# Performance work log

Hardware: AMD Instinct MI355X
Metric: run time of the kernel (lower is better)

Reference implementation:

```python
import jax, jax.numpy as jnp
import numpy as np
from jax import lax

DIM = 192
NUM_CLASSES = 4
D_INNER = 2 * DIM          # expand=2
D_STATE = 16
D_CONV = 4
DT_RANK = (DIM + 15) // 16  # ceil(192/16)=12
PATCH = 16


def _mamba_params(key, prefix):
    ks = jax.random.split(key, 9)
    s = lambda k, shape, scale: (jax.random.normal(k, shape, jnp.float32) * scale)
    p = {
        prefix + '_in_w':   s(ks[0], (2 * D_INNER, DIM), 0.02),
        prefix + '_conv_w': s(ks[1], (D_INNER, D_CONV), 0.1),
        prefix + '_conv_b': jnp.zeros((D_INNER,), jnp.float32),
        prefix + '_xproj_w': s(ks[2], (DT_RANK + 2 * D_STATE, D_INNER), 0.02),
        prefix + '_dt_w':   s(ks[3], (D_INNER, DT_RANK), 0.1),
        prefix + '_dt_b':   s(ks[4], (D_INNER,), 0.1),
        # A_log init: log(1..d_state) broadcast over d_inner (mamba default)
        prefix + '_A_log':  jnp.broadcast_to(jnp.log(jnp.arange(1, D_STATE + 1, dtype=jnp.float32)), (D_INNER, D_STATE)) + 0.0,
        prefix + '_D':      jnp.ones((D_INNER,), jnp.float32),
        prefix + '_out_w':  s(ks[5], (DIM, D_INNER), 0.02),
    }
    return p


def setup_inputs() -> dict:
    key = jax.random.key(0)
    ks = jax.random.split(key, 8)
    inp = {
        'x': jax.random.normal(ks[0], (32, 3, 384, 384), jnp.float32),
        'patch_w': jax.random.normal(ks[1], (DIM, 3, PATCH, PATCH), jnp.float32) * 0.02,
        'patch_b': jnp.zeros((DIM,), jnp.float32),
        'ln_g': jnp.ones((DIM,), jnp.float32),
        'ln_b': jnp.zeros((DIM,), jnp.float32),
        'fc_w': jax.random.normal(ks[2], (NUM_CLASSES, DIM), jnp.float32) * 0.02,
        'fc_b': jnp.zeros((NUM_CLASSES,), jnp.float32),
    }
    inp.update(_mamba_params(ks[3], 'f'))
    inp.update(_mamba_params(ks[4], 'b'))
    return inp


def _layernorm(x, g, b, eps=1e-5):
    mu = jnp.mean(x, -1, keepdims=True)
    var = jnp.mean(jnp.square(x - mu), -1, keepdims=True)
    return (x - mu) * lax.rsqrt(var + eps) * g + b


def _mamba(x, in_w, conv_w, conv_b, xproj_w, dt_w, dt_b, A_log, Dskip, out_w):
    # x: [B, L, DIM]
    Bn, L, _ = x.shape
    xz = x @ in_w.T                                    # [B, L, 2*di]
    xi, z = jnp.split(xz, 2, axis=-1)
    # causal depthwise conv1d, kernel D_CONV, left pad
    xp = jnp.pad(xi, ((0, 0), (D_CONV - 1, 0), (0, 0)))
    xc = conv_b + sum(xp[:, k:k + L, :] * conv_w[:, k] for k in range(D_CONV))
    xc = jax.nn.silu(xc)                               # [B, L, di]
    proj = xc @ xproj_w.T                              # [B, L, dtr+2*ds]
    dt, Bm, Cm = jnp.split(proj, [DT_RANK, DT_RANK + D_STATE], axis=-1)
    dt = jax.nn.softplus(dt @ dt_w.T + dt_b)           # [B, L, di]
    A = -jnp.exp(A_log)                                # [di, ds]

    def step(h, inp):
        dt_t, B_t, C_t, x_t = inp                      # [B,di],[B,ds],[B,ds],[B,di]
        dA = jnp.exp(dt_t[:, :, None] * A)             # [B, di, ds]
        h = dA * h + (dt_t * x_t)[:, :, None] * B_t[:, None, :]
        y = jnp.einsum('bds,bs->bd', h, C_t)
        return h, y

    h0 = jnp.zeros((Bn, D_INNER, D_STATE), x.dtype)
    xs = (dt.transpose(1, 0, 2), Bm.transpose(1, 0, 2),
          Cm.transpose(1, 0, 2), xc.transpose(1, 0, 2))
    _, ys = lax.scan(step, h0, xs)                     # [L, B, di]
    y = ys.transpose(1, 0, 2) + xc * Dskip
    y = y * jax.nn.silu(z)
    return y @ out_w.T                                 # [B, L, DIM]


def reference(x, patch_w, patch_b, ln_g, ln_b, fc_w, fc_b,
              f_in_w, f_conv_w, f_conv_b, f_xproj_w, f_dt_w, f_dt_b, f_A_log, f_D, f_out_w,
              b_in_w, b_conv_w, b_conv_b, b_xproj_w, b_dt_w, b_dt_b, b_A_log, b_D, b_out_w):
    Bn, C, H, W = x.shape
    Hp, Wp = H // PATCH, W // PATCH
    # patch embed: stride==kernel conv == reshape + einsum
    xr = x.reshape(Bn, C, Hp, PATCH, Wp, PATCH)
    tok = jnp.einsum('bchpwq,dcpq->bhwd', xr, patch_w) + patch_b
    tok = tok.reshape(Bn, Hp * Wp, DIM)                # [B, L, D]
    tok = _layernorm(tok, ln_g, ln_b)
    fwd = _mamba(tok, f_in_w, f_conv_w, f_conv_b, f_xproj_w, f_dt_w, f_dt_b, f_A_log, f_D, f_out_w)
    bwd = _mamba(tok[:, ::-1, :], b_in_w, b_conv_w, b_conv_b, b_xproj_w, b_dt_w, b_dt_b, b_A_log, b_D, b_out_w)
    out = fwd + bwd[:, ::-1, :]
    pooled = jnp.mean(out, axis=1)                     # adaptive avg pool to 1
    return pooled @ fc_w.T + fc_b                      # [B, num_classes]
```

## Files before the change

kernel.cpp:

```cpp
#include <hip/hip_runtime.h>
#include <hip/hip_bf16.h>

#define NC 32
#define CL 18

typedef __attribute__((ext_vector_type(8))) short short8;
typedef __attribute__((ext_vector_type(4))) float f32x4;
typedef __attribute__((ext_vector_type(2))) float f32x2;

__device__ __forceinline__ float sigm(float x){ return 1.0f/(1.0f+__expf(-x)); }

__device__ __forceinline__ ushort f2bf(float f){
  unsigned u = __float_as_uint(f);
  unsigned r = (u + 0x7fffu + ((u>>16)&1u)) >> 16;
  return (ushort)r;
}
__device__ __forceinline__ float bf2f(ushort h){ return __uint_as_float(((unsigned)h)<<16); }

__global__ __launch_bounds__(256) void k_prep_all(
    const float* __restrict__ patch_w, const float* __restrict__ f_in_w,
    const float* __restrict__ b_in_w,
    const float* __restrict__ f_xw, const float* __restrict__ b_xw,
    const float* __restrict__ f_cw, const float* __restrict__ b_cw,
    const float* __restrict__ f_al, const float* __restrict__ b_al,
    const float* __restrict__ fc_w, const float* __restrict__ f_ow,
    const float* __restrict__ b_ow,
    ushort* __restrict__ pw_h, ushort* __restrict__ pw_l,
    ushort* __restrict__ iw_h, ushort* __restrict__ iw_l,
    ushort* __restrict__ xw_h, ushort* __restrict__ xw_l,
    float* __restrict__ cwT, float* __restrict__ Abuf,
    float* __restrict__ A0fl, float* __restrict__ W2){
  const int bx = blockIdx.x, t = threadIdx.x;
  if (bx < 1728){
    int which = bx/576;
    int i = (bx - which*576)*256 + t;
    if (which==0){
      float f = patch_w[i];
      ushort hb = f2bf(f);
      pw_h[i]=hb; pw_l[i]=f2bf(f - bf2f(hb));
    } else {
      const float* src = (which==1) ? f_in_w : b_in_w;
      int dirofs = (which==1) ? 0 : 48;
      float f = src[i];
      int n = i/192, k = i%192;
      int nblk = n>>4, r = n&15, kblk = k>>5, kk = k&31;
      int lane = r + ((kk>>3)<<4), j = kk&7;
      size_t idx = ((size_t)((nblk+dirofs)*6 + kblk)*64 + lane)*8 + j;
      ushort hb = f2bf(f);
      iw_h[idx]=hb; iw_l[idx]=f2bf(f - bf2f(hb));
    }
  } else if (bx < 1872){
    int i = (bx-1728)*256 + t;
    int dir=i/(48*384), rem=i%(48*384), n=rem/384, k=rem%384;
    float v = (n<44) ? (dir?b_xw:f_xw)[n*384+k] : 0.f;
    ushort hb = f2bf(v);
    xw_h[i]=hb; xw_l[i]=f2bf(v - bf2f(hb));
  } else if (bx < 1884){
    int i = (bx-1872)*256 + t;
    int dir=i/1536, rem=i%1536, j=rem/384, k=rem%384;
    cwT[i] = (dir ? b_cw : f_cw)[k*4+j];
  } else if (bx < 1887){
    int i = (bx-1884)*256 + t;
    if (i < 768){
      int dir=i/384, di=i%384;
      const float* alp = (dir?b_al:f_al) + di*16;
      float A0 = -expf(alp[0]);
      bool fast = true;
      Abuf[(size_t)i*16] = A0;
      #pragma unroll
      for (int s=1;s<16;s++){
        float A = -expf(alp[s]);
        Abuf[(size_t)i*16+s] = A;
        fast = fast && (fabsf(A - (s+1)*A0) <= 1e-5f*(s+1)*fabsf(A0));
      }
      A0fl[i*2]=A0; A0fl[i*2+1]=fast?1.f:0.f;
    }
  } else {
    int i = (bx-1887)*256 + t;
    if (i < 768){
      int dir=i/384, di=i%384;
      const float* ow = dir ? b_ow : f_ow;
      float a0=0.f,a1=0.f,a2=0.f,a3=0.f;
      for (int d=0; d<192; ++d){
        float o = ow[d*384 + di];
        a0 += fc_w[0*192+d]*o; a1 += fc_w[1*192+d]*o;
        a2 += fc_w[2*192+d]*o; a3 += fc_w[3*192+d]*o;
      }
      W2[(0*2+dir)*384+di]=a0; W2[(1*2+dir)*384+di]=a1;
      W2[(2*2+dir)*384+di]=a2; W2[(3*2+dir)*384+di]=a3;
    }
  }
}
__device__ __forceinline__ float w2at(const float* W2, int dir, int ch, int di){
  return W2[(ch*2+dir)*384+di];
}

__global__ __launch_bounds__(1024) void k_patch(
    const float* __restrict__ x,
    const ushort* __restrict__ pw_h, const ushort* __restrict__ pw_l,
    const float* __restrict__ pb, const float* __restrict__ lng,
    const float* __restrict__ lnb,
    ushort* __restrict__ tokf_h, ushort* __restrict__ tokf_l,
    int b0, int Mc){
  __shared__ __align__(16) char sBmem[49152];
  __shared__ __align__(16) ushort sAh[64*64], sAl[64*64];
  __shared__ float sLN[4][64][2];
  ushort* sBh = (ushort*)sBmem;
  ushort* sBl = (ushort*)(sBmem + 24576);
  const int tid = threadIdx.x;
  const int m0 = blockIdx.x*64;
  const int lane = tid&63, w = tid>>6;
  const int wr = w>>2, wc = w&3;
  const int r = lane&15, g = lane>>4;
  f32x4 acc[3];
  #pragma unroll
  for (int i=0;i<3;i++) acc[i] = (f32x4){0.f,0.f,0.f,0.f};

  for (int s=0;s<12;s++){
    const int c = s>>2, p0 = (s&3)*4;
    {
      int f = tid;
      int m = f>>4, rem = f&15, pp = rem>>2, qq = rem&3;
      int rm = m0 + m;
      float4 v = make_float4(0.f,0.f,0.f,0.f);
      if (rm < Mc){
        int b = b0 + rm/576, l = rm%576, hp = l/24, wp = l%24;
        size_t idx4 = ((size_t)((b*3+c)*384) + hp*16 + p0+pp)*96 + wp*4 + qq;
        v = reinterpret_cast<const float4*>(x)[idx4];
      }
      ushort4 hv, lv;
      hv.x=f2bf(v.x); lv.x=f2bf(v.x-bf2f(hv.x));
      hv.y=f2bf(v.y); lv.y=f2bf(v.y-bf2f(hv.y));
      hv.z=f2bf(v.z); lv.z=f2bf(v.z-bf2f(hv.z));
      hv.w=f2bf(v.w); lv.w=f2bf(v.w-bf2f(hv.w));
      int byte = (m*128 + pp*32 + qq*8) ^ ((m&7)<<4);
      *reinterpret_cast<ushort4*>((char*)sAh + byte) = hv;
      *reinterpret_cast<ushort4*>((char*)sAl + byte) = lv;
    }
    #pragma unroll
    for (int i=0;i<2;i++){
      int f = tid + i*1024;
      if (f < 1536){
        int n = f>>3, k8 = f&7;
        size_t gi = (size_t)n*768 + s*64 + k8*8;
        uint4 bh = *reinterpret_cast<const uint4*>(pw_h + gi);
        uint4 bl = *reinterpret_cast<const uint4*>(pw_l + gi);
        int byte = (n*128 + k8*16) ^ ((n&7)<<4);
        *reinterpret_cast<uint4*>((char*)sBh + byte) = bh;
        *reinterpret_cast<uint4*>((char*)sBl + byte) = bl;
      }
    }
    __syncthreads();
    #pragma unroll
    for (int kk=0;kk<2;kk++){
      int arow = wr*16 + r;
      int abyte = (arow*128 + kk*64 + g*16) ^ ((arow&7)<<4);
      short8 ah = *reinterpret_cast<const short8*>((char*)sAh + abyte);
      short8 al = *reinterpret_cast<const short8*>((char*)sAl + abyte);
      #pragma unroll
      for (int nfl=0; nfl<3; nfl++){
        int brow = (wc*3+nfl)*16 + r;
        int bbyte = (brow*128 + kk*64 + g*16) ^ ((brow&7)<<4);
        short8 bh = *reinterpret_cast<const short8*>((char*)sBh + bbyte);
        short8 bll = *reinterpret_cast<const short8*>((char*)sBl + bbyte);
        acc[nfl] = __builtin_amdgcn_mfma_f32_16x16x32_bf16(ah, bh, acc[nfl], 0,0,0);
        acc[nfl] = __builtin_amdgcn_mfma_f32_16x16x32_bf16(ah, bll, acc[nfl], 0,0,0);
        acc[nfl] = __builtin_amdgcn_mfma_f32_16x16x32_bf16(al, bh, acc[nfl], 0,0,0);
      }
    }
    __syncthreads();
  }
  float pbv[3], gv[3], bv[3];
  #pragma unroll
  for (int nfl=0;nfl<3;nfl++){
    int col = (wc*3+nfl)*16 + r;
    pbv[nfl]=pb[col]; gv[nfl]=lng[col]; bv[nfl]=lnb[col];
  }
  #pragma unroll
  for (int nfl=0;nfl<3;nfl++)
    #pragma unroll
    for (int q=0;q<4;q++) acc[nfl][q] += pbv[nfl];
  float sum[4]={0,0,0,0}, sq[4]={0,0,0,0};
  #pragma unroll
  for (int nfl=0;nfl<3;nfl++)
    #pragma unroll
    for (int q=0;q<4;q++){ float v=acc[nfl][q]; sum[q]+=v; sq[q]+=v*v; }
  #pragma unroll
  for (int off=1; off<16; off<<=1){
    #pragma unroll
    for (int q=0;q<4;q++){
      sum[q]+=__shfl_xor(sum[q],off);
      sq[q] +=__shfl_xor(sq[q],off);
    }
  }
  if (r==0){
    #pragma unroll
    for (int q=0;q<4;q++){
      int row = wr*16 + g*4 + q;
      sLN[wc][row][0]=sum[q]; sLN[wc][row][1]=sq[q];
    }
  }
  __syncthreads();
  float* sT = (float*)sBmem;
  #pragma unroll
  for (int q=0;q<4;q++){
    int rl = wr*16 + g*4 + q;
    float stot = sLN[0][rl][0]+sLN[1][rl][0]+sLN[2][rl][0]+sLN[3][rl][0];
    float qtot = sLN[0][rl][1]+sLN[1][rl][1]+sLN[2][rl][1]+sLN[3][rl][1];
    float mu = stot*(1.f/192.f);
    float var = qtot*(1.f/192.f) - mu*mu;
    float rs = rsqrtf(var + 1e-5f);
    #pragma unroll
    for (int nfl=0;nfl<3;nfl++)
      sT[rl*192 + (wc*3+nfl)*16 + r] = (acc[nfl][q]-mu)*rs*gv[nfl] + bv[nfl];
  }
  __syncthreads();
  const int mB = m0>>4;
  #pragma unroll
  for (int i=0;i<2;i++){
    int fl = tid + 1024*i;
    if (fl < 1536){
      int mb = fl/384, rem = fl-mb*384, kb = rem>>6, ln = rem&63;
      int rr = ln&15, gq = ln>>4;
      const float* sp = sT + (mb*16+rr)*192 + kb*32 + gq*8;
      short8 hv, lv;
      #pragma unroll
      for (int j=0;j<8;j++){
        float v = sp[j];
        ushort hb = f2bf(v);
        hv[j] = (short)hb;
        lv[j] = (short)f2bf(v - bf2f(hb));
      }
      size_t o = ((size_t)((mB+mb)*6 + kb)*64 + ln)*8;
      *reinterpret_cast<short8*>(tokf_h + o) = hv;
      *reinterpret_cast<short8*>(tokf_l + o) = lv;
    }
  }
}

__global__ __launch_bounds__(1024) void k_inproj(
    const ushort* __restrict__ tokf_h, const ushort* __restrict__ tokf_l,
    const ushort* __restrict__ iw_h, const ushort* __restrict__ iw_l,
    float* __restrict__ xib, ushort* __restrict__ zb, int Bc, int Mc){
  __shared__ __align__(16) char sMem[65536];
  ushort* sAh = (ushort*)sMem;
  ushort* sAl = (ushort*)(sMem + 16384);
  ushort* sBh = (ushort*)(sMem + 32768);
  ushort* sBl = (ushort*)(sMem + 49152);
  const int tid = threadIdx.x;
  const int lane = tid&63, w = tid>>6;
  const int wr = w>>2, wc = w&3;
  const int r = lane&15, g = lane>>4;
  const int m0 = blockIdx.x*128;
  const int mb0 = blockIdx.x*8;
  const int nb0 = blockIdx.y*8;
  const int n0d = (blockIdx.y%6)*128;
  const bool dir1 = (blockIdx.y >= 6);
  const bool isZ = ((blockIdx.y%6) >= 3);

  f32x4 acc[2][2];
  #pragma unroll
  for (int a=0;a<2;a++)
    #pragma unroll
    for (int b=0;b<2;b++) acc[a][b] = (f32x4){0.f,0.f,0.f,0.f};

  for (int s=0;s<3;s++){
    {
      const int f = w;
      const int mf = f>>1, kk = f&1;
      const size_t ga = ((size_t)((mb0+mf)*6 + 2*s+kk)*64 + lane)*8;
      const size_t gb = ((size_t)((nb0+mf)*6 + 2*s+kk)*64 + lane)*8;
      const int so = f*512 + lane*8;
      *reinterpret_cast<short8*>(sAh+so) = *reinterpret_cast<const short8*>(tokf_h+ga);
      *reinterpret_cast<short8*>(sBh+so) = *reinterpret_cast<const short8*>(iw_h+gb);
      if (!isZ){
        *reinterpret_cast<short8*>(sAl+so) = *reinterpret_cast<const short8*>(tokf_l+ga);
        *reinterpret_cast<short8*>(sBl+so) = *reinterpret_cast<const short8*>(iw_l+gb);
      }
    }
    __syncthreads();
    #pragma unroll
    for (int kk=0;kk<2;kk++){
      short8 ah[2], al[2];
      #pragma unroll
      for (int mf=0;mf<2;mf++){
        const int fo = ((wr*2+mf)*2+kk)*512 + lane*8;
        ah[mf] = *reinterpret_cast<const short8*>(sAh+fo);
        if (!isZ) al[mf] = *reinterpret_cast<const short8*>(sAl+fo);
      }
      #pragma unroll
      for (int nf=0;nf<2;nf++){
        const int fo = ((wc*2+nf)*2+kk)*512 + lane*8;
        short8 bh = *reinterpret_cast<const short8*>(sBh+fo);
        if (isZ){
          #pragma unroll
          for (int mf=0;mf<2;mf++)
            acc[mf][nf] = __builtin_amdgcn_mfma_f32_16x16x32_bf16(ah[mf], bh, acc[mf][nf], 0,0,0);
        } else {
          short8 bl = *reinterpret_cast<const short8*>(sBl+fo);
          #pragma unroll
          for (int mf=0;mf<2;mf++){
            acc[mf][nf] = __builtin_amdgcn_mfma_f32_16x16x32_bf16(ah[mf], bh, acc[mf][nf], 0,0,0);
            acc[mf][nf] = __builtin_amdgcn_mfma_f32_16x16x32_bf16(ah[mf], bl, acc[mf][nf], 0,0,0);
            acc[mf][nf] = __builtin_amdgcn_mfma_f32_16x16x32_bf16(al[mf], bh, acc[mf][nf], 0,0,0);
          }
        }
      }
    }
    __syncthreads();
  }

  float* sT = reinterpret_cast<float*>(sMem);
  const int h_of_w = wr>>1;
  #pragma unroll
  for (int h=0; h<2; h++){
    if (h==1) __syncthreads();
    if (h_of_w == h){
      #pragma unroll
      for (int mf=0;mf<2;mf++)
        #pragma unroll
        for (int nf=0;nf<2;nf++)
          #pragma unroll
          for (int q=0;q<4;q++){
            int rl = (wr&1)*32 + mf*16 + g*4 + q;
            int c  = wc*32 + nf*16 + r;
            sT[rl*132 + c] = acc[mf][nf][q];
          }
    }
    __syncthreads();
    {
      const int rl = tid>>4, cg = tid&15;
      const int rm = m0 + h*64 + rl;
      if (rm < Mc){
        size_t row;
        if (dir1){
          int bl = rm/576, l = rm - bl*576;
          row = (size_t)(Bc + bl)*576 + (575-l);
        } else {
          row = (size_t)rm;
        }
        const float* sp = sT + rl*132 + cg*8;
        if (!isZ){
          *reinterpret_cast<f32x4*>(xib + row*384 + n0d + cg*8)     = *reinterpret_cast<const f32x4*>(sp);
          *reinterpret_cast<f32x4*>(xib + row*384 + n0d + cg*8 + 4) = *reinterpret_cast<const f32x4*>(sp+4);
        } else {
          short8 hv;
          #pragma unroll
          for (int j=0;j<8;j++){
            float v = sp[j];
            v = v*sigm(v);
            hv[j] = (short)f2bf(v);
          }
          *reinterpret_cast<short8*>(zb + row*384 + (n0d-384) + cg*8) = hv;
        }
      }
    }
  }
}

__global__ __launch_bounds__(256) void k_convx(
    const float* __restrict__ xib, const float* __restrict__ cwT,
    const float* __restrict__ f_cb, const float* __restrict__ b_cb,
    const ushort* __restrict__ xw_h, const ushort* __restrict__ xw_l,
    float* __restrict__ proj, ushort* __restrict__ xcb, int Bc){
  __shared__ __align__(16) float sRaw[67*64];
  __shared__ __align__(16) ushort sAh[64*64], sAl[64*64];
  __shared__ __align__(16) ushort sBh[48*64], sBl[48*64];
  const int dir = blockIdx.z, blk = blockIdx.y, l0 = blockIdx.x*64;
  const int tid = threadIdx.x, lane = tid&63, w = tid>>6;
  const int r = lane&15, g = lane>>4;
  const size_t seq = ((size_t)dir*Bc + blk)*576;
  const float* cwTd = cwT + dir*1536;
  const float* cbp  = dir?b_cb:f_cb;
  const ushort* bhp = xw_h + dir*48*384;
  const ushort* blp = xw_l + dir*48*384;
  f32x4 acc[3];
  #pragma unroll
  for (int i=0;i<3;i++) acc[i] = (f32x4){0.f,0.f,0.f,0.f};

  for (int kc=0; kc<6; ++kc){
    #pragma unroll
    for (int i=0;i<5;i++){
      int f = tid + i*256;
      if (f < 67*16){
        int rr = f>>4, kq = f&15;
        int l = l0 + rr - 3;
        float4 v = make_float4(0.f,0.f,0.f,0.f);
        if (l >= 0) v = *reinterpret_cast<const float4*>(xib + (seq+l)*384 + kc*64 + kq*4);
        int kqs = kq ^ (rr&15);
        *reinterpret_cast<float4*>(sRaw + rr*64 + kqs*4) = v;
      }
    }
    __syncthreads();
    #pragma unroll
    for (int i=0;i<4;i++){
      int f = tid + i*256;
      int m = f>>4, kq = f&15;
      float4 a = reinterpret_cast<const float4*>(cbp)[kc*16 + kq];
      #pragma unroll
      for (int j=0;j<4;j++){
        int rr = m + j;
        float4 rv = *reinterpret_cast<const float4*>(sRaw + rr*64 + (kq ^ (rr&15))*4);
        float4 cv = reinterpret_cast<const float4*>(cwTd)[j*96 + kc*16 + kq];
        a.x += cv.x*rv.x; a.y += cv.y*rv.y; a.z += cv.z*rv.z; a.w += cv.w*rv.w;
      }
      a.x = a.x*sigm(a.x); a.y = a.y*sigm(a.y); a.z = a.z*sigm(a.z); a.w = a.w*sigm(a.w);
      ushort4 hv, lv;
      hv.x=f2bf(a.x); lv.x=f2bf(a.x-bf2f(hv.x));
      hv.y=f2bf(a.y); lv.y=f2bf(a.y-bf2f(hv.y));
      hv.z=f2bf(a.z); lv.z=f2bf(a.z-bf2f(hv.z));
      hv.w=f2bf(a.w); lv.w=f2bf(a.w-bf2f(hv.w));
      *reinterpret_cast<ushort4*>(xcb + (seq + l0 + m)*384 + kc*64 + kq*4) = hv;
      int byte = (m*128 + kq*8) ^ ((m&7)<<4);
      *reinterpret_cast<ushort4*>((char*)sAh + byte) = hv;
      *reinterpret_cast<ushort4*>((char*)sAl + byte) = lv;
    }
    #pragma unroll
    for (int i=0;i<2;i++){
      int f = tid + i*256;
      if (f < 384){
        int n = f>>3, k8 = f&7;
        size_t gi = (size_t)n*384 + kc*64 + k8*8;
        uint4 vh = *reinterpret_cast<const uint4*>(bhp + gi);
        uint4 vl = *reinterpret_cast<const uint4*>(blp + gi);
        int byte = (n*128 + k8*16) ^ ((n&7)<<4);
        *reinterpret_cast<uint4*>((char*)sBh + byte) = vh;
        *reinterpret_cast<uint4*>((char*)sBl + byte) = vl;
      }
    }
    __syncthreads();
    #pragma unroll
    for (int kk=0;kk<2;kk++){
      int arow = w*16 + r;
      int abyte = (arow*128 + kk*64 + g*16) ^ ((arow&7)<<4);
      short8 ah = *reinterpret_cast<const short8*>((char*)sAh + abyte);
      short8 al = *reinterpret_cast<const short8*>((char*)sAl + abyte);
      #pragma unroll
      for (int nf=0;nf<3;nf++){
        int brow = nf*16 + r;
        int bbyte = (brow*128 + kk*64 + g*16) ^ ((brow&7)<<4);
        short8 bh = *reinterpret_cast<const short8*>((char*)sBh + bbyte);
        short8 bll = *reinterpret_cast<const short8*>((char*)sBl + bbyte);
        acc[nf] = __builtin_amdgcn_mfma_f32_16x16x32_bf16(ah, bh, acc[nf], 0,0,0);
        acc[nf] = __builtin_amdgcn_mfma_f32_16x16x32_bf16(ah, bll, acc[nf], 0,0,0);
        acc[nf] = __builtin_amdgcn_mfma_f32_16x16x32_bf16(al, bh, acc[nf], 0,0,0);
      }
    }
    __syncthreads();
  }
  #pragma unroll
  for (int nf=0;nf<3;nf++){
    int col = nf*16 + r;
    if (col < 44){
      #pragma unroll
      for (int q=0;q<4;q++){
        int l = l0 + w*16 + g*4 + q;
        proj[(seq+l)*44 + col] = acc[nf][q];
      }
    }
  }
}

__global__ __launch_bounds__(256) void k_scan_p1(
    const ushort* __restrict__ zb, const ushort* __restrict__ xcb,
    const float* __restrict__ proj,
    const float* __restrict__ f_dtw, const float* __restrict__ b_dtw,
    const float* __restrict__ f_dtb, const float* __restrict__ b_dtb,
    const float* __restrict__ A0fl, const float* __restrict__ Abuf,
    const float* __restrict__ f_D,  const float* __restrict__ b_D,
    const float* __restrict__ W2, float* __restrict__ dtend,
    float* __restrict__ hbuf, float* __restrict__ part, int b0, int Bc){
  const int dir=blockIdx.z, bl=blockIdx.y;
  const int gg=blockIdx.x>>3, cq=blockIdx.x&7;
  const int wv=threadIdx.x>>6, lane=threadIdx.x&63;
  const int c = cq*4 + wv;
  const int di = gg*64 + lane;
  const size_t seq = ((size_t)dir*Bc + bl)*576;
  const float* dtwp = (dir?b_dtw:f_dtw) + di*12;
  float dtw[12];
  #pragma unroll
  for (int i=0;i<3;i++){
    float4 t = reinterpret_cast<const float4*>(dtwp)[i];
    dtw[4*i]=t.x; dtw[4*i+1]=t.y; dtw[4*i+2]=t.z; dtw[4*i+3]=t.w;
  }
  float dtb = (dir?b_dtb:f_dtb)[di];
  float2 af = reinterpret_cast<const float2*>(A0fl)[dir*384+di];
  const float A0 = af.x;
  const bool fast = (af.y != 0.f);
  float A[16];
  if (!fast){
    #pragma unroll
    for (int s=0;s<16;s++) A[s] = Abuf[((size_t)dir*384+di)*16+s];
  }
  float Dv = (dir?b_D:f_D)[di];
  float w2c[4];
  #pragma unroll
  for (int ch=0;ch<4;ch++) w2c[ch] = w2at(W2,dir,ch,di);
  f32x2 h2[8];
  #pragma unroll
  for (int p=0;p<8;p++) h2[p]=(f32x2){0.f,0.f};
  float S=0.f, cum=0.f;
  const int l0 = c*CL;
  const int pbase = (int)((seq + (size_t)l0)*44);
  const ushort* xcp = xcb + di;
  const ushort* zbp2 = zb + di;
  for (int j=0;j<CL;j++){
    const size_t row = seq + l0 + j;
    const int po = __builtin_amdgcn_readfirstlane(pbase + j*44);
    const float4* pr4 = reinterpret_cast<const float4*>(proj + po);
    float4 t0=pr4[0], t1=pr4[1], t2=pr4[2];
    float dtin = dtb
      + t0.x*dtw[0]+t0.y*dtw[1]+t0.z*dtw[2]+t0.w*dtw[3]
      + t1.x*dtw[4]+t1.y*dtw[5]+t1.z*dtw[6]+t1.w*dtw[7]
      + t2.x*dtw[8]+t2.y*dtw[9]+t2.z*dtw[10]+t2.w*dtw[11];
    float dt = (dtin > 20.f) ? dtin : __logf(1.f + __expf(dtin));
    cum += dt;
    float xc = bf2f(xcp[row*384]);
    float zs = bf2f(zbp2[row*384]);
    float u = dt*xc;
    f32x2 u2 = {u,u};
    f32x2 dA2[8];
    if (fast){
      float e1=__expf(dt*A0);
      float e2=e1*e1;
      f32x2 e2v={e2,e2};
      dA2[0]=(f32x2){e1,e2};
      #pragma unroll
      for (int p=1;p<8;p++) dA2[p]=dA2[p-1]*e2v;
    } else {
      #pragma unroll
      for (int p=0;p<8;p++){
        dA2[p]=(f32x2){__expf(dt*A[2*p]), __expf(dt*A[2*p+1])};
      }
    }
    f32x2 ya={0.f,0.f}, yb={0.f,0.f};
    #pragma unroll
    for (int i=0;i<4;i++){
      float4 tb=pr4[3+i], tc=pr4[7+i];
      f32x2 B0={tb.x,tb.y}, B1={tb.z,tb.w};
      f32x2 C0={tc.x,tc.y}, C1={tc.z,tc.w};
      h2[2*i]   = dA2[2*i]*h2[2*i]     + u2*B0;
      h2[2*i+1] = dA2[2*i+1]*h2[2*i+1] + u2*B1;
      ya += h2[2*i]*C0;
      yb += h2[2*i+1]*C1;
    }
    S += ((ya[0]+ya[1])+(yb[0]+yb[1]) + xc*Dv)*zs;
  }
  dtend[(((size_t)dir*Bc + bl)*NC + c)*384 + di] = cum;
  size_t hb = ((((size_t)c*2+dir)*Bc + bl)*6 + gg)*1024;
  #pragma unroll
  for (int s=0;s<16;s++) hbuf[hb + s*64 + lane] = h2[s>>1][s&1];
  float p0=S*w2c[0], p1v=S*w2c[1], p2v=S*w2c[2], p3v=S*w2c[3];
  #pragma unroll
  for (int off=32; off>0; off>>=1){
    p0 += __shfl_xor(p0, off); p1v += __shfl_xor(p1v, off);
    p2v += __shfl_xor(p2v, off); p3v += __shfl_xor(p3v, off);
  }
  if (lane==0){
    float* dst = part + ((((size_t)dir*32 + (b0+bl))*6 + gg)*64 + c)*4;
    dst[0]=p0; dst[1]=p1v; dst[2]=p2v; dst[3]=p3v;
  }
}

__global__ __launch_bounds__(256) void k_combine(
    const float* __restrict__ dtend, float* __restrict__ hbuf,
    const float* __restrict__ A0fl, const float* __restrict__ Abuf, int Bc){
  const int gg=blockIdx.x, bl=blockIdx.y, dir=blockIdx.z;
  const int wv=threadIdx.x>>6, lane=threadIdx.x&63, di=gg*64+lane;
  float2 af = reinterpret_cast<const float2*>(A0fl)[dir*384+di];
  const bool fast = (af.y != 0.f);
  float Aeff[4];
  #pragma unroll
  for (int si=0;si<4;si++){
    int s = wv*4+si;
    Aeff[si] = fast ? af.x*(float)(s+1) : Abuf[((size_t)dir*384+di)*16+s];
  }
  float cur[4];
  size_t hx0 = ((((size_t)0*2+dir)*Bc+bl)*6+gg)*1024 + (wv*4)*64 + lane;
  #pragma unroll
  for (int si=0;si<4;si++) cur[si]=hbuf[hx0 + si*64];
  for (int c=1;c<NC;c++){
    size_t hx=((((size_t)c*2+dir)*Bc+bl)*6+gg)*1024 + (wv*4)*64 + lane;
    float tmp[4];
    #pragma unroll
    for (int si=0;si<4;si++){ tmp[si]=hbuf[hx+si*64]; hbuf[hx+si*64]=cur[si]; }
    if (c<NC-1){
      float Sdt = dtend[(((size_t)dir*Bc+bl)*NC + c)*384 + di];
      #pragma unroll
      for (int si=0;si<4;si++) cur[si] = __expf(Aeff[si]*Sdt)*cur[si] + tmp[si];
    }
  }
}

__global__ __launch_bounds__(256) void k_scan_p2(
    const ushort* __restrict__ zb, const float* __restrict__ proj,
    const float* __restrict__ hbuf,
    const float* __restrict__ f_dtw, const float* __restrict__ b_dtw,
    const float* __restrict__ f_dtb, const float* __restrict__ b_dtb,
    const float* __restrict__ A0fl, const float* __restrict__ Abuf,
    const float* __restrict__ W2, float* __restrict__ part, int b0, int Bc){
  const int dir=blockIdx.z, bl=blockIdx.y;
  const int gg=blockIdx.x>>3, cq=blockIdx.x&7;
  const int wv=threadIdx.x>>6, lane=threadIdx.x&63;
  const int c = cq*4 + wv + 1;
  const int di = gg*64 + lane;
  const size_t seq = ((size_t)dir*Bc + bl)*576;
  if (c >= NC) return;
  const float* dtwp = (dir?b_dtw:f_dtw) + di*12;
  float dtw[12];
  #pragma unroll
  for (int i=0;i<3;i++){
    float4 t = reinterpret_cast<const float4*>(dtwp)[i];
    dtw[4*i]=t.x; dtw[4*i+1]=t.y; dtw[4*i+2]=t.z; dtw[4*i+3]=t.w;
  }
  float dtb = (dir?b_dtb:f_dtb)[di];
  float2 af = reinterpret_cast<const float2*>(A0fl)[dir*384+di];
  const float A0 = af.x;
  const bool fast = (af.y != 0.f);
  float A[16];
  if (!fast){
    #pragma unroll
    for (int s=0;s<16;s++) A[s] = Abuf[((size_t)dir*384+di)*16+s];
  }
  float w2c[4];
  #pragma unroll
  for (int ch=0;ch<4;ch++) w2c[ch]=w2at(W2,dir,ch,di);
  f32x2 hh2[8];
  size_t hb=((((size_t)c*2+dir)*Bc+bl)*6+gg)*1024;
  #pragma unroll
  for (int s=0;s<16;s++) hh2[s>>1][s&1]=hbuf[hb+s*64+lane];
  float S=0.f;
  const int l0 = c*CL;
  const int pbase = (int)((seq + (size_t)l0)*44);
  const ushort* zbp2 = zb + di;
  for (int j=0;j<CL;j++){
    const size_t row = seq + l0 + j;
    const int po = __builtin_amdgcn_readfirstlane(pbase + j*44);
    const float4* pr4 = reinterpret_cast<const float4*>(proj + po);
    float4 t0=pr4[0], t1=pr4[1], t2=pr4[2];
    float dtin = dtb
      + t0.x*dtw[0]+t0.y*dtw[1]+t0.z*dtw[2]+t0.w*dtw[3]
      + t1.x*dtw[4]+t1.y*dtw[5]+t1.z*dtw[6]+t1.w*dtw[7]
      + t2.x*dtw[8]+t2.y*dtw[9]+t2.z*dtw[10]+t2.w*dtw[11];
    float dt = (dtin > 20.f) ? dtin : __logf(1.f + __expf(dtin));
    float zs = bf2f(zbp2[row*384]);
    f32x2 dA2[8];
    if (fast){
      float e1=__expf(dt*A0);
      float e2=e1*e1;
      f32x2 e2v={e2,e2};
      dA2[0]=(f32x2){e1,e2};
      #pragma unroll
      for (int p=1;p<8;p++) dA2[p]=dA2[p-1]*e2v;
    } else {
      #pragma unroll
      for (int p=0;p<8;p++){
        dA2[p]=(f32x2){__expf(dt*A[2*p]), __expf(dt*A[2*p+1])};
      }
    }
    f32x2 ya={0.f,0.f}, yb={0.f,0.f};
    #pragma unroll
    for (int i=0;i<4;i++){
      float4 tc = pr4[7+i];
      f32x2 C0={tc.x,tc.y}, C1={tc.z,tc.w};
      hh2[2*i]   = hh2[2*i]*dA2[2*i];
      hh2[2*i+1] = hh2[2*i+1]*dA2[2*i+1];
      ya += hh2[2*i]*C0;
      yb += hh2[2*i+1]*C1;
    }
    S += ((ya[0]+ya[1])+(yb[0]+yb[1]))*zs;
  }
  float p0=S*w2c[0], p1v=S*w2c[1], p2v=S*w2c[2], p3v=S*w2c[3];
  #pragma unroll
  for (int off=32; off>0; off>>=1){
    p0 += __shfl_xor(p0, off); p1v += __shfl_xor(p1v, off);
    p2v += __shfl_xor(p2v, off); p3v += __shfl_xor(p3v, off);
  }
  if (lane==0){
    float* dst = part + ((((size_t)dir*32 + (b0+bl))*6 + gg)*64 + 32 + c)*4;
    dst[0]=p0; dst[1]=p1v; dst[2]=p2v; dst[3]=p3v;
  }
}

__global__ __launch_bounds__(256) void k_final(const float* __restrict__ part,
                                               const float* __restrict__ fc_b,
                                               float* __restrict__ out){
  const int b = blockIdx.x;
  const int ch = threadIdx.x>>6, lane = threadIdx.x&63;
  float s = 0.f;
  for (int i = lane; i < 768; i += 64){
    int c = i & 63;
    if (c == 32) continue;
    int dg = i >> 6;
    int dir = dg >= 6 ? 1 : 0;
    int g = dg - dir*6;
    s += part[((((size_t)dir*32 + b)*6 + g)*64 + c)*4 + ch];
  }
  #pragma unroll
  for (int off=32; off>0; off>>=1) s += __shfl_xor(s, off);
  if (lane==0) out[b*4+ch] = fc_b[ch] + s*(1.0f/576.0f);
}

extern "C" void kernel_launch(void* const* d_in, const int* in_sizes, int n_in,
                              void* d_out, int out_size, void* d_ws, size_t ws_size,
                              hipStream_t stream){
  const float* x       = (const float*)d_in[0];
  const float* patch_w = (const float*)d_in[1];
  const float* patch_b = (const float*)d_in[2];
  const float* ln_g    = (const float*)d_in[3];
  const float* ln_b    = (const float*)d_in[4];
  const float* fc_w    = (const float*)d_in[5];
  const float* fc_b    = (const float*)d_in[6];
  const float* f_in_w  = (const float*)d_in[7];
  const float* f_cw    = (const float*)d_in[8];
  const float* f_cb    = (const float*)d_in[9];
  const float* f_xw    = (const float*)d_in[10];
  const float* f_dtw   = (const float*)d_in[11];
  const float* f_dtb   = (const float*)d_in[12];
  const float* f_al    = (const float*)d_in[13];
  const float* f_D     = (const float*)d_in[14];
  const float* f_ow    = (const float*)d_in[15];
  const float* b_in_w  = (const float*)d_in[16];
  const float* b_cw    = (const float*)d_in[17];
  const float* b_cb    = (const float*)d_in[18];
  const float* b_xw    = (const float*)d_in[19];
  const float* b_dtw   = (const float*)d_in[20];
  const float* b_dtb   = (const float*)d_in[21];
  const float* b_al    = (const float*)d_in[22];
  const float* b_D     = (const float*)d_in[23];
  const float* b_ow    = (const float*)d_in[24];
  float* out = (float*)d_out;
  float* ws  = (float*)d_ws;

  float* W2    = ws;
  float* part  = W2 + 3072;
  ushort* pw_h = (ushort*)(part + 98304);
  ushort* pw_l = pw_h + 147456;
  ushort* iw_h = pw_l + 147456;
  ushort* iw_l = iw_h + 294912;
  ushort* xw_h = iw_l + 294912;
  ushort* xw_l = xw_h + 36864;
  float* cwT   = (float*)(xw_l + 36864);
  float* Abuf  = cwT + 3072;
  float* A0fl  = Abuf + 12288;
  float* base  = A0fl + 1536;

  const size_t FIXED = 3072 + 98304 + 2*73728 + 2*147456 + 2*18432 + 3072
                     + 12288 + 1536;
  const size_t perB = 110592ull + 442368ull + 110592ull + 110592ull
                    + 24576ull + 393216ull;
  int Bc = 32;
  while (Bc > 1 && (FIXED + (size_t)Bc*perB)*4ull > ws_size) Bc >>= 1;

  ushort* tokf_h = (ushort*)base;
  ushort* tokf_l = tokf_h + (size_t)Bc*110592ull;
  float* prj  = base;
  float* xib  = base + (size_t)Bc*110592ull;
  ushort* zbp = (ushort*)(xib + (size_t)Bc*442368ull);
  ushort* xcb = zbp + (size_t)Bc*442368ull;
  float* dtnd = (float*)(xcb + (size_t)Bc*442368ull);
  float* hbf  = dtnd + (size_t)Bc*24576ull;

  k_prep_all<<<dim3(1890),dim3(256),0,stream>>>(patch_w, f_in_w, b_in_w,
                                                f_xw, b_xw, f_cw, b_cw,
                                                f_al, b_al, fc_w, f_ow, b_ow,
                                                pw_h, pw_l, iw_h, iw_l,
                                                xw_h, xw_l, cwT, Abuf, A0fl, W2);

  for (int b0=0; b0<32; b0+=Bc){
    const int Mc = Bc*576;
    k_patch<<<dim3((Mc+63)/64),dim3(1024),0,stream>>>(x, pw_h, pw_l, patch_b,
                                                      ln_g, ln_b, tokf_h, tokf_l, b0, Mc);
    k_inproj<<<dim3((Mc+127)/128,12),dim3(1024),0,stream>>>(tokf_h, tokf_l, iw_h, iw_l,
                                                            xib, zbp, Bc, Mc);
    k_convx<<<dim3(9,Bc,2),dim3(256),0,stream>>>(xib, cwT, f_cb, b_cb,
                                                 xw_h, xw_l, prj, xcb, Bc);
    k_scan_p1<<<dim3(48,Bc,2),dim3(256),0,stream>>>(zbp, xcb, prj,
                                                    f_dtw,b_dtw, f_dtb,b_dtb,
                                                    A0fl, Abuf, f_D,b_D,
                                                    W2, dtnd, hbf, part, b0, Bc);
    k_combine<<<dim3(6,Bc,2),dim3(256),0,stream>>>(dtnd, hbf, A0fl, Abuf, Bc);
    k_scan_p2<<<dim3(48,Bc,2),dim3(256),0,stream>>>(zbp, prj, hbf,
                                                    f_dtw,b_dtw, f_dtb,b_dtb,
                                                    A0fl, Abuf, W2, part, b0, Bc);
  }
  k_final<<<dim3(32),dim3(256),0,stream>>>(part, fc_b, out);
}
```

Measured before the change: 238.2 us.

## Restructure chunked selective scan into four long chunks and prefetch patch-embed tiles

The chunked scan goes from 32 chunks of 18 steps to 4 chunks of 144 steps. Each block now covers all 384 channels of one chunk, and the combine and second-pass kernels are rewritten to match. This cuts the cross-chunk combine and recompute overhead and the size of the partial buffers, but leaves far fewer blocks (4*Bc*2 in the first pass) and much longer serial loops. Separately, the patch-embedding GEMM register-prefetches the next k-slice of x and the weights while computing the current one, to hide global load latency.

After: 336.9 us. 1.41x slower.

```diff
diff --git a/kernel.cpp b/kernel.cpp
--- a/kernel.cpp
+++ b/kernel.cpp
@@ -1,8 +1,8 @@
 #include <hip/hip_runtime.h>
 #include <hip/hip_bf16.h>
 
-#define NC 32
-#define CL 18
+#define NC4 4
+#define CL4 144
 
 typedef __attribute__((ext_vector_type(8))) short short8;
 typedef __attribute__((ext_vector_type(4))) float f32x4;
@@ -116,41 +116,65 @@
   #pragma unroll
   for (int i=0;i<3;i++) acc[i] = (f32x4){0.f,0.f,0.f,0.f};
 
+  const int mA = tid>>4, remA = tid&15, ppA = remA>>2, qqA = remA&3;
+  const int rmA = m0 + mA;
+  const bool okA = (rmA < Mc);
+  size_t baseA = 0;
+  if (okA){
+    int b = b0 + rmA/576, l = rmA%576, hp = l/24, wp = l%24;
+    baseA = ((size_t)(b*3)*384 + hp*16 + ppA)*96 + wp*4 + qqA;
+  }
+  const int nB0 = tid>>3, k8B0 = tid&7;
+  const bool okB1 = (tid < 512);
+  const int fB1 = tid + 1024;
+  const int nB1 = fB1>>3, k8B1 = fB1&7;
+  const int byteA  = (mA*128 + ppA*32 + qqA*8) ^ ((mA&7)<<4);
+  const int byteB0 = (nB0*128 + k8B0*16) ^ ((nB0&7)<<4);
+  const int byteB1 = (nB1*128 + k8B1*16) ^ ((nB1&7)<<4);
+
+  float4 vA = make_float4(0.f,0.f,0.f,0.f);
+  uint4 vBh0 = {}, vBl0 = {}, vBh1 = {}, vBl1 = {};
+  {
+    if (okA) vA = reinterpret_cast<const float4*>(x)[baseA];
+    size_t gi0 = (size_t)nB0*768 + k8B0*8;
+    vBh0 = *reinterpret_cast<const uint4*>(pw_h + gi0);
+    vBl0 = *reinterpret_cast<const uint4*>(pw_l + gi0);
+    if (okB1){
+      size_t gi1 = (size_t)nB1*768 + k8B1*8;
+      vBh1 = *reinterpret_cast<const uint4*>(pw_h + gi1);
+      vBl1 = *reinterpret_cast<const uint4*>(pw_l + gi1);
+    }
+  }
+
   for (int s=0;s<12;s++){
-    const int c = s>>2, p0 = (s&3)*4;
     {
-      int f = tid;
-      int m = f>>4, rem = f&15, pp = rem>>2, qq = rem&3;
-      int rm = m0 + m;
-      float4 v = make_float4(0.f,0.f,0.f,0.f);
-      if (rm < Mc){
-        int b = b0 + rm/576, l = rm%576, hp = l/24, wp = l%24;
-        size_t idx4 = ((size_t)((b*3+c)*384) + hp*16 + p0+pp)*96 + wp*4 + qq;
-        v = reinterpret_cast<const float4*>(x)[idx4];
-      }
       ushort4 hv, lv;
-      hv.x=f2bf(v.x); lv.x=f2bf(v.x-bf2f(hv.x));
-      hv.y=f2bf(v.y); lv.y=f2bf(v.y-bf2f(hv.y));
-      hv.z=f2bf(v.z); lv.z=f2bf(v.z-bf2f(hv.z));
-      hv.w=f2bf(v.w); lv.w=f2bf(v.w-bf2f(hv.w));
-      int byte = (m*128 + pp*32 + qq*8) ^ ((m&7)<<4);
-      *reinterpret_cast<ushort4*>((char*)sAh + byte) = hv;
-      *reinterpret_cast<ushort4*>((char*)sAl + byte) = lv;
-    }
-    #pragma unroll
-    for (int i=0;i<2;i++){
-      int f = tid + i*1024;
-      if (f < 1536){
-        int n = f>>3, k8 = f&7;
-        size_t gi = (size_t)n*768 + s*64 + k8*8;
-        uint4 bh = *reinterpret_cast<const uint4*>(pw_h + gi);
-        uint4 bl = *reinterpret_cast<const uint4*>(pw_l + gi);
-        int byte = (n*128 + k8*16) ^ ((n&7)<<4);
-        *reinterpret_cast<uint4*>((char*)sBh + byte) = bh;
-        *reinterpret_cast<uint4*>((char*)sBl + byte) = bl;
+      hv.x=f2bf(vA.x); lv.x=f2bf(vA.x-bf2f(hv.x));
+      hv.y=f2bf(vA.y); lv.y=f2bf(vA.y-bf2f(hv.y));
+      hv.z=f2bf(vA.z); lv.z=f2bf(vA.z-bf2f(hv.z));
+      hv.w=f2bf(vA.w); lv.w=f2bf(vA.w-bf2f(hv.w));
+      *reinterpret_cast<ushort4*>((char*)sAh + byteA) = hv;
+      *reinterpret_cast<ushort4*>((char*)sAl + byteA) = lv;
+      *reinterpret_cast<uint4*>((char*)sBh + byteB0) = vBh0;
+      *reinterpret_cast<uint4*>((char*)sBl + byteB0) = vBl0;
+      if (okB1){
+        *reinterpret_cast<uint4*>((char*)sBh + byteB1) = vBh1;
+        *reinterpret_cast<uint4*>((char*)sBl + byteB1) = vBl1;
       }
     }
     __syncthreads();
+    if (s < 11){
+      int s1 = s+1, c1 = s1>>2, p01 = (s1&3)*4;
+      if (okA) vA = reinterpret_cast<const float4*>(x)[baseA + ((size_t)c1*384 + p01)*96];
+      size_t gi0 = (size_t)nB0*768 + (size_t)s1*64 + k8B0*8;
+      vBh0 = *reinterpret_cast<const uint4*>(pw_h + gi0);
+      vBl0 = *reinterpret_cast<const uint4*>(pw_l + gi0);
+      if (okB1){
+        size_t gi1 = (size_t)nB1*768 + (size_t)s1*64 + k8B1*8;
+        vBh1 = *reinterpret_cast<const uint4*>(pw_h + gi1);
+        vBl1 = *reinterpret_cast<const uint4*>(pw_l + gi1);
+      }
+    }
     #pragma unroll
     for (int kk=0;kk<2;kk++){
       int arow = wr*16 + r;
@@ -461,20 +485,18 @@
   }
 }
 
-__global__ __launch_bounds__(256) void k_scan_p1(
+__global__ __launch_bounds__(384) void k_scan1(
     const ushort* __restrict__ zb, const ushort* __restrict__ xcb,
     const float* __restrict__ proj,
     const float* __restrict__ f_dtw, const float* __restrict__ b_dtw,
     const float* __restrict__ f_dtb, const float* __restrict__ b_dtb,
     const float* __restrict__ A0fl, const float* __restrict__ Abuf,
     const float* __restrict__ f_D,  const float* __restrict__ b_D,
-    const float* __restrict__ W2, float* __restrict__ dtend,
-    float* __restrict__ hbuf, float* __restrict__ part, int b0, int Bc){
-  const int dir=blockIdx.z, bl=blockIdx.y;
-  const int gg=blockIdx.x>>3, cq=blockIdx.x&7;
-  const int wv=threadIdx.x>>6, lane=threadIdx.x&63;
-  const int c = cq*4 + wv;
-  const int di = gg*64 + lane;
+    const float* __restrict__ W2, float* __restrict__ dtnd,
+    float* __restrict__ hend, float* __restrict__ part, int b0, int Bc){
+  const int c = blockIdx.x, bl = blockIdx.y, dir = blockIdx.z;
+  const int di = threadIdx.x;
+  const int w = di>>6, lane = di&63;
   const size_t seq = ((size_t)dir*Bc + bl)*576;
   const float* dtwp = (dir?b_dtw:f_dtw) + di*12;
   float dtw[12];
@@ -500,11 +522,11 @@
   #pragma unroll
   for (int p=0;p<8;p++) h2[p]=(f32x2){0.f,0.f};
   float S=0.f, cum=0.f;
-  const int l0 = c*CL;
+  const int l0 = c*CL4;
   const int pbase = (int)((seq + (size_t)l0)*44);
   const ushort* xcp = xcb + di;
   const ushort* zbp2 = zb + di;
-  for (int j=0;j<CL;j++){
+  for (int j=0;j<CL4;j++){
     const size_t row = seq + l0 + j;
     const int po = __builtin_amdgcn_readfirstlane(pbase + j*44);
     const float4* pr4 = reinterpret_cast<const float4*>(proj + po);
@@ -546,10 +568,13 @@
     }
     S += ((ya[0]+ya[1])+(yb[0]+yb[1]) + xc*Dv)*zs;
   }
-  dtend[(((size_t)dir*Bc + bl)*NC + c)*384 + di] = cum;
-  size_t hb = ((((size_t)c*2+dir)*Bc + bl)*6 + gg)*1024;
-  #pragma unroll
-  for (int s=0;s<16;s++) hbuf[hb + s*64 + lane] = h2[s>>1][s&1];
+  if (c==1 || c==2)
+    dtnd[(((size_t)dir*Bc + bl)*4 + c)*384 + di] = cum;
+  if (c < 3){
+    size_t hb = (((size_t)(c*2+dir)*Bc + bl)*16)*384 + di;
+    #pragma unroll
+    for (int s=0;s<16;s++) hend[hb + (size_t)s*384] = h2[s>>1][s&1];
+  }
   float p0=S*w2c[0], p1v=S*w2c[1], p2v=S*w2c[2], p3v=S*w2c[3];
   #pragma unroll
   for (int off=32; off>0; off>>=1){
@@ -557,55 +582,55 @@
     p2v += __shfl_xor(p2v, off); p3v += __shfl_xor(p3v, off);
   }
   if (lane==0){
-    float* dst = part + ((((size_t)dir*32 + (b0+bl))*6 + gg)*64 + c)*4;
+    float* dst = part + ((((size_t)dir*32 + (b0+bl))*4 + c)*6 + w)*4;
     dst[0]=p0; dst[1]=p1v; dst[2]=p2v; dst[3]=p3v;
   }
 }
 
-__global__ __launch_bounds__(256) void k_combine(
-    const float* __restrict__ dtend, float* __restrict__ hbuf,
-    const float* __restrict__ A0fl, const float* __restrict__ Abuf, int Bc){
-  const int gg=blockIdx.x, bl=blockIdx.y, dir=blockIdx.z;
-  const int wv=threadIdx.x>>6, lane=threadIdx.x&63, di=gg*64+lane;
+__global__ __launch_bounds__(384) void k_comb4(
+    const float* __restrict__ dtnd, const float* __restrict__ hend,
+    const float* __restrict__ A0fl, const float* __restrict__ Abuf,
+    float* __restrict__ h0b, int Bc){
+  const int bl = blockIdx.x, dir = blockIdx.y;
+  const int di = threadIdx.x;
   float2 af = reinterpret_cast<const float2*>(A0fl)[dir*384+di];
   const bool fast = (af.y != 0.f);
-  float Aeff[4];
-  #pragma unroll
-  for (int si=0;si<4;si++){
-    int s = wv*4+si;
-    Aeff[si] = fast ? af.x*(float)(s+1) : Abuf[((size_t)dir*384+di)*16+s];
-  }
-  float cur[4];
-  size_t hx0 = ((((size_t)0*2+dir)*Bc+bl)*6+gg)*1024 + (wv*4)*64 + lane;
-  #pragma unroll
-  for (int si=0;si<4;si++) cur[si]=hbuf[hx0 + si*64];
-  for (int c=1;c<NC;c++){
-    size_t hx=((((size_t)c*2+dir)*Bc+bl)*6+gg)*1024 + (wv*4)*64 + lane;
-    float tmp[4];
-    #pragma unroll
-    for (int si=0;si<4;si++){ tmp[si]=hbuf[hx+si*64]; hbuf[hx+si*64]=cur[si]; }
-    if (c<NC-1){
-      float Sdt = dtend[(((size_t)dir*Bc+bl)*NC + c)*384 + di];
-      #pragma unroll
-      for (int si=0;si<4;si++) cur[si] = __expf(Aeff[si]*Sdt)*cur[si] + tmp[si];
-    }
-  }
-}
-
-__global__ __launch_bounds__(256) void k_scan_p2(
+  float As[16];
+  #pragma unroll
+  for (int s=0;s<16;s++)
+    As[s] = fast ? af.x*(float)(s+1) : Abuf[((size_t)dir*384+di)*16+s];
+  float H[16];
+  {
+    size_t hb = (((size_t)(0*2+dir)*Bc + bl)*16)*384 + di;
+    #pragma unroll
+    for (int s=0;s<16;s++) H[s] = hend[hb + (size_t)s*384];
+    size_t ob = (((size_t)(0*2+dir)*Bc + bl)*16)*384 + di;
+    #pragma unroll
+    for (int s=0;s<16;s++) h0b[ob + (size_t)s*384] = H[s];
+  }
+  for (int cc=1; cc<3; ++cc){
+    float cum = dtnd[(((size_t)dir*Bc + bl)*4 + cc)*384 + di];
+    size_t hb = (((size_t)(cc*2+dir)*Bc + bl)*16)*384 + di;
+    #pragma unroll
+    for (int s=0;s<16;s++)
+      H[s] = __expf(As[s]*cum)*H[s] + hend[hb + (size_t)s*384];
+    size_t ob = (((size_t)(cc*2+dir)*Bc + bl)*16)*384 + di;
+    #pragma unroll
+    for (int s=0;s<16;s++) h0b[ob + (size_t)s*384] = H[s];
+  }
+}
+
+__global__ __launch_bounds__(384) void k_scan2(
     const ushort* __restrict__ zb, const float* __restrict__ proj,
-    const float* __restrict__ hbuf,
+    const float* __restrict__ h0b,
     const float* __restrict__ f_dtw, const float* __restrict__ b_dtw,
     const float* __restrict__ f_dtb, const float* __restrict__ b_dtb,
     const float* __restrict__ A0fl, const float* __restrict__ Abuf,
-    const float* __restrict__ W2, float* __restrict__ part, int b0, int Bc){
-  const int dir=blockIdx.z, bl=blockIdx.y;
-  const int gg=blockIdx.x>>3, cq=blockIdx.x&7;
-  const int wv=threadIdx.x>>6, lane=threadIdx.x&63;
-  const int c = cq*4 + wv + 1;
-  const int di = gg*64 + lane;
+    const float* __restrict__ W2, float* __restrict__ part2, int b0, int Bc){
+  const int c = blockIdx.x + 1, bl = blockIdx.y, dir = blockIdx.z;
+  const int di = threadIdx.x;
+  const int w = di>>6, lane = di&63;
   const size_t seq = ((size_t)dir*Bc + bl)*576;
-  if (c >= NC) return;
   const float* dtwp = (dir?b_dtw:f_dtw) + di*12;
   float dtw[12];
   #pragma unroll
@@ -626,14 +651,16 @@
   #pragma unroll
   for (int ch=0;ch<4;ch++) w2c[ch]=w2at(W2,dir,ch,di);
   f32x2 hh2[8];
-  size_t hb=((((size_t)c*2+dir)*Bc+bl)*6+gg)*1024;
-  #pragma unroll
-  for (int s=0;s<16;s++) hh2[s>>1][s&1]=hbuf[hb+s*64+lane];
+  {
+    size_t hb = (((size_t)((c-1)*2+dir)*Bc + bl)*16)*384 + di;
+    #pragma unroll
+    for (int s=0;s<16;s++) hh2[s>>1][s&1] = h0b[hb + (size_t)s*384];
+  }
   float S=0.f;
-  const int l0 = c*CL;
+  const int l0 = c*CL4;
   const int pbase = (int)((seq + (size_t)l0)*44);
   const ushort* zbp2 = zb + di;
-  for (int j=0;j<CL;j++){
+  for (int j=0;j<CL4;j++){
     const size_t row = seq + l0 + j;
     const int po = __builtin_amdgcn_readfirstlane(pbase + j*44);
     const float4* pr4 = reinterpret_cast<const float4*>(proj + po);
@@ -677,24 +704,27 @@
     p2v += __shfl_xor(p2v, off); p3v += __shfl_xor(p3v, off);
   }
   if (lane==0){
-    float* dst = part + ((((size_t)dir*32 + (b0+bl))*6 + gg)*64 + 32 + c)*4;
+    float* dst = part2 + ((((size_t)dir*32 + (b0+bl))*3 + (c-1))*6 + w)*4;
     dst[0]=p0; dst[1]=p1v; dst[2]=p2v; dst[3]=p3v;
   }
 }
 
 __global__ __launch_bounds__(256) void k_final(const float* __restrict__ part,
+                                               const float* __restrict__ part2,
                                                const float* __restrict__ fc_b,
                                                float* __restrict__ out){
   const int b = blockIdx.x;
   const int ch = threadIdx.x>>6, lane = threadIdx.x&63;
   float s = 0.f;
-  for (int i = lane; i < 768; i += 64){
-    int c = i & 63;
-    if (c == 32) continue;
-    int dg = i >> 6;
-    int dir = dg >= 6 ? 1 : 0;
-    int g = dg - dir*6;
-    s += part[((((size_t)dir*32 + b)*6 + g)*64 + c)*4 + ch];
+  if (lane < 48){
+    int dir = lane/24, rem = lane - dir*24;
+    int c = rem/6, w = rem - c*6;
+    s += part[((((size_t)dir*32 + b)*4 + c)*6 + w)*4 + ch];
+  }
+  if (lane < 36){
+    int dir = lane/18, rem = lane - dir*18;
+    int c1 = rem/6, w = rem - c1*6;
+    s += part2[((((size_t)dir*32 + b)*3 + c1)*6 + w)*4 + ch];
   }
   #pragma unroll
   for (int off=32; off>0; off>>=1) s += __shfl_xor(s, off);
@@ -734,7 +764,8 @@
 
   float* W2    = ws;
   float* part  = W2 + 3072;
-  ushort* pw_h = (ushort*)(part + 98304);
+  float* part2 = part + 6144;
+  ushort* pw_h = (ushort*)(part2 + 4608);
   ushort* pw_l = pw_h + 147456;
   ushort* iw_h = pw_l + 147456;
   ushort* iw_l = iw_h + 294912;
@@ -745,10 +776,8 @@
   float* A0fl  = Abuf + 12288;
   float* base  = A0fl + 1536;
 
-  const size_t FIXED = 3072 + 98304 + 2*73728 + 2*147456 + 2*18432 + 3072
-                     + 12288 + 1536;
-  const size_t perB = 110592ull + 442368ull + 110592ull + 110592ull
-                    + 24576ull + 393216ull;
+  const size_t FIXED = 509952ull;
+  const size_t perB  = 1072128ull;
   int Bc = 32;
   while (Bc > 1 && (FIXED + (size_t)Bc*perB)*4ull > ws_size) Bc >>= 1;
 
@@ -759,7 +788,8 @@
   ushort* zbp = (ushort*)(xib + (size_t)Bc*442368ull);
   ushort* xcb = zbp + (size_t)Bc*442368ull;
   float* dtnd = (float*)(xcb + (size_t)Bc*442368ull);
-  float* hbf  = dtnd + (size_t)Bc*24576ull;
+  float* hend = dtnd + (size_t)Bc*3072ull;
+  float* h0b  = hend + (size_t)Bc*36864ull;
 
   k_prep_all<<<dim3(1890),dim3(256),0,stream>>>(patch_w, f_in_w, b_in_w,
                                                 f_xw, b_xw, f_cw, b_cw,
@@ -775,14 +805,14 @@
                                                             xib, zbp, Bc, Mc);
     k_convx<<<dim3(9,Bc,2),dim3(256),0,stream>>>(xib, cwT, f_cb, b_cb,
                                                  xw_h, xw_l, prj, xcb, Bc);
-    k_scan_p1<<<dim3(48,Bc,2),dim3(256),0,stream>>>(zbp, xcb, prj,
-                                                    f_dtw,b_dtw, f_dtb,b_dtb,
-                                                    A0fl, Abuf, f_D,b_D,
-                                                    W2, dtnd, hbf, part, b0, Bc);
-    k_combine<<<dim3(6,Bc,2),dim3(256),0,stream>>>(dtnd, hbf, A0fl, Abuf, Bc);
-    k_scan_p2<<<dim3(48,Bc,2),dim3(256),0,stream>>>(zbp, prj, hbf,
-                                                    f_dtw,b_dtw, f_dtb,b_dtb,
-                                                    A0fl, Abuf, W2, part, b0, Bc);
-  }
-  k_final<<<dim3(32),dim3(256),0,stream>>>(part, fc_b, out);
-}
+    k_scan1<<<dim3(4,Bc,2),dim3(384),0,stream>>>(zbp, xcb, prj,
+                                                 f_dtw,b_dtw, f_dtb,b_dtb,
+                                                 A0fl, Abuf, f_D,b_D,
+                                                 W2, dtnd, hend, part, b0, Bc);
+    k_comb4<<<dim3(Bc,2),dim3(384),0,stream>>>(dtnd, hend, A0fl, Abuf, h0b, Bc);
+    k_scan2<<<dim3(3,Bc,2),dim3(384),0,stream>>>(zbp, prj, h0b,
+                                                 f_dtw,b_dtw, f_dtb,b_dtb,
+                                                 A0fl, Abuf, W2, part2, b0, Bc);
+  }
+  k_final<<<dim3(32),dim3(256),0,stream>>>(part, part2, fc_b, out);
+}
```
